# Kernel optimization log

Measured on AMD Instinct MI355X. Metric: run time of the kernel, lower is better.

The kernel has to match this reference:

```python
import jax, jax.numpy as jnp
import numpy as np

EPS = 0.001  # additive floor applied after relu, as in the torch code


def setup_inputs() -> dict:
    key = jax.random.key(0)
    kA, kB, kW = jax.random.split(key, 3)
    M, N, C, H, W = 512, 64, 128, 8, 8
    A = jax.random.normal(kA, (M, C, H, W), dtype=jnp.float32)
    B = jax.random.normal(kB, (N, C, H, W), dtype=jnp.float32)
    Wg = jax.random.normal(kW, (C, C), dtype=jnp.float32) * 0.01  # Wg.data.normal_(0.0, 0.01)
    return {"A": A, "B": B, "Wg": Wg}


def reference(A, B, Wg):
    # Faithful vectorization of MIMOcom.get_source_dst_max(A, B, dir=True).
    # Torch loops i,j over HxW: B0 = B[:, i, j, :]; G = B0 @ Wg;
    # combination[m, n, p] = sum_c A[m, p, c] * G[n, c]; running max over (i, j).
    M, C, H, W = A.shape
    N = B.shape[0]
    P = H * W
    Af = jnp.transpose(A, (0, 2, 3, 1)).reshape(M, P, C)  # [M, P, C]
    Bf = jnp.transpose(B, (0, 2, 3, 1)).reshape(N, P, C)  # [N, Q, C]
    G = Bf @ Wg                                           # [N, Q, D]
    scores = jnp.einsum('mpd,nqd->mnpq', Af, G)           # [M, N, P, Q]
    comb_max = scores.max(axis=-1)                        # max over B positions q
    return jax.nn.relu(comb_max) + EPS                    # [M, N, P]
```

## Files before the change

kernel.cpp:

```cpp
#include <hip/hip_runtime.h>
#include <hip/hip_bf16.h>
#include <stdint.h>

typedef __attribute__((ext_vector_type(8))) short bf16x8;
typedef __attribute__((ext_vector_type(16))) float f32x16;
using bf16 = __hip_bfloat16;

static constexpr int Mdim = 512;
static constexpr int Ndim = 64;
static constexpr int Cdim = 128;
static constexpr int Pdim = 64;
static constexpr float EPS_ADD = 0.001f;

#define SB0 __builtin_amdgcn_sched_barrier(0)

__global__ void prep_kernel(const float* __restrict__ A, const float* __restrict__ B,
                            const float* __restrict__ Wg,
                            bf16* __restrict__ Afrag, bf16* __restrict__ Gfrag) {
    __shared__ float lds[128 * 65];
    const int t = threadIdx.x;

    if (blockIdx.x < 512) {
        const int m = blockIdx.x;
        const float* __restrict__ Am = A + (size_t)m * (Cdim * Pdim);
#pragma unroll
        for (int i = 0; i < 8; ++i) {
            int v = t + i * 256;
            int gidx = v * 4;
            int c = gidx >> 6, p = gidx & 63;
            float4 val = *reinterpret_cast<const float4*>(Am + gidx);
            float* dst = &lds[c * 65 + p];
            dst[0] = val.x; dst[1] = val.y; dst[2] = val.z; dst[3] = val.w;
        }
        __syncthreads();

        unsigned* __restrict__ dst32 = (unsigned*)(Afrag + (size_t)m * 8192);
#pragma unroll
        for (int i = 0; i < 16; ++i) {
            int pr = t + i * 256;
            int p = pr >> 6;
            int c = (pr & 63) << 1;
            float f0 = lds[c * 65 + p];
            float f1 = lds[(c + 1) * 65 + p];
            union { bf16 hh[2]; unsigned u; } pk;
            pk.hh[0] = __float2bfloat16(f0);
            pk.hh[1] = __float2bfloat16(f1);
            int h = p >> 5, l31 = p & 31;
            int ks = c >> 4, hi = (c >> 3) & 1, e = c & 7;
            dst32[h * 2048 + ks * 256 + hi * 128 + l31 * 4 + (e >> 1)] = pk.u;
        }
    } else {
        const int nb = blockIdx.x - 512;
        const int n  = nb >> 2;
        const int q0 = (nb & 3) * 16;
        const float* __restrict__ Bn = B + (size_t)n * (Cdim * Pdim);
#pragma unroll
        for (int i = 0; i < 8; ++i) {
            int v = t + i * 256;
            int gidx = v * 4;
            int c = gidx >> 6, q = gidx & 63;
            float4 val = *reinterpret_cast<const float4*>(Bn + gidx);
            float* dst = &lds[c * 65 + q];
            dst[0] = val.x; dst[1] = val.y; dst[2] = val.z; dst[3] = val.w;
        }
        __syncthreads();

        const int d  = t & 127;
        const int qb = q0 + (t >> 7) * 8;
        float acc[8] = {0.f, 0.f, 0.f, 0.f, 0.f, 0.f, 0.f, 0.f};
        for (int c = 0; c < 128; ++c) {
            float w = Wg[c * 128 + d];
#pragma unroll
            for (int qi = 0; qi < 8; ++qi)
                acc[qi] = fmaf(lds[c * 65 + qb + qi], w, acc[qi]);
        }
        bf16* __restrict__ gdst = Gfrag + (size_t)n * 8192;
        const int ks = d >> 4, hi = (d >> 3) & 1, e = d & 7;
#pragma unroll
        for (int qi = 0; qi < 8; ++qi) {
            int q = qb + qi;
            int qt = q >> 5, l31 = q & 31;
            gdst[qt * 4096 + ks * 512 + hi * 256 + l31 * 8 + e] = __float2bfloat16(acc[qi]);
        }
    }
}

__global__ __launch_bounds__(256, 2)
void gemm_max_kernel(const bf16* __restrict__ Afrag, const bf16* __restrict__ Gfrag,
                     float* __restrict__ out) {
    const int tid  = threadIdx.x;
    const int lane = tid & 63;
    const int w    = tid >> 6;
    const int nw = w >> 1, h = w & 1;
    const int l31 = lane & 31, hi = lane >> 5;
    const int mg = blockIdx.x & 31;
    const int bn = blockIdx.x >> 5;
    const int n  = bn * 2 + nw;
    const int phase = bn & 15;

    bf16x8 gf[2][8];
    {
        const bf16* Gp = Gfrag + (size_t)n * 8192 + lane * 8;
#pragma unroll
        for (int qt = 0; qt < 2; ++qt)
#pragma unroll
            for (int ks = 0; ks < 8; ++ks)
                gf[qt][ks] = *reinterpret_cast<const bf16x8*>(Gp + qt * 4096 + ks * 512);
    }

    const bf16* Ab = Afrag + (size_t)mg * 16 * 8192 + h * 4096 + lane * 8;
    auto loadA = [&](bf16x8 (&dst)[8], int se) {
        const bf16* p = Ab + (size_t)se * 8192;
#pragma unroll
        for (int ks = 0; ks < 8; ++ks)
            dst[ks] = *reinterpret_cast<const bf16x8*>(p + ks * 512);
    };

    f32x16 acc0, acc1;
    const f32x16 z16 = {0.f,0.f,0.f,0.f,0.f,0.f,0.f,0.f,0.f,0.f,0.f,0.f,0.f,0.f,0.f,0.f};

    auto compute = [&](const bf16x8 (&a)[8]) {
#pragma unroll
        for (int ks = 0; ks < 8; ++ks) {
            acc0 = __builtin_amdgcn_mfma_f32_32x32x16_bf16(
                gf[0][ks], a[ks], ks == 0 ? z16 : acc0, 0, 0, 0);
            acc1 = __builtin_amdgcn_mfma_f32_32x32x16_bf16(
                gf[1][ks], a[ks], ks == 0 ? z16 : acc1, 0, 0, 0);
        }
    };

    auto epilogue = [&](int se) {
        float v01 = fmaxf(acc0[0], acc0[1]);
#pragma unroll
        for (int j = 2; j < 16; ++j) v01 = fmaxf(v01, acc0[j]);
        float v23 = fmaxf(acc1[0], acc1[1]);
#pragma unroll
        for (int j = 2; j < 16; ++j) v23 = fmaxf(v23, acc1[j]);
        float v = fmaxf(v01, v23);
        v = fmaxf(v, __shfl_xor(v, 32));
        if (hi == 0)
            out[(size_t)(mg * 16 + se) * 4096 + n * 64 + h * 32 + l31] =
                fmaxf(v, 0.f) + EPS_ADD;
    };

    bf16x8 aA[8], aB[8];
    loadA(aA, phase);

#pragma unroll
    for (int s = 0; s < 16; ++s) {
        const int se = (s + phase) & 15;
        const int sn = (s + 1 + phase) & 15;
        if ((s & 1) == 0) {
            if (s < 15) loadA(aB, sn);
            SB0;
            compute(aA);
            epilogue(se);
        } else {
            if (s < 15) loadA(aA, sn);
            SB0;
            compute(aB);
            epilogue(se);
        }
    }
}

extern "C" void kernel_launch(void* const* d_in, const int* in_sizes, int n_in,
                              void* d_out, int out_size, void* d_ws, size_t ws_size,
                              hipStream_t stream) {
    const float* A  = (const float*)d_in[0];
    const float* B  = (const float*)d_in[1];
    const float* Wg = (const float*)d_in[2];
    float* out = (float*)d_out;

    bf16* Afrag = (bf16*)d_ws;
    bf16* Gfrag = (bf16*)((char*)d_ws + (size_t)Mdim * Pdim * Cdim * sizeof(bf16));

    prep_kernel<<<768, 256, 0, stream>>>(A, B, Wg, Afrag, Gfrag);
    gemm_max_kernel<<<1024, 256, 0, stream>>>(Afrag, Gfrag, out);
}
```

Before: 55.83 us.

## Keep A fragments in registers and stream shared G tiles through LDS

The GEMM-max kernel is restructured so that each wave keeps one row m of A (both P halves) in registers and loops over 16 values of n. The G fragments for those n are staged into a double-buffered LDS tile with global_load_lds and shared by the block's four waves, instead of each wave reloading A from global memory. Synchronisation uses explicit vmcnt waits plus barriers, the grid is halved, and each step now issues four MFMAs per k-slice. The aim is less global/L2 traffic and better reuse of G. In exchange the kernel uses more LDS, and it depends on vmcnt ordering with the output stores.

```diff
diff --git a/kernel.cpp b/kernel.cpp
--- a/kernel.cpp
+++ b/kernel.cpp
@@ -13,6 +13,15 @@
 static constexpr float EPS_ADD = 0.001f;
 
 #define SB0 __builtin_amdgcn_sched_barrier(0)
+#define WAITV(N) asm volatile("s_waitcnt vmcnt(" #N ")" ::: "memory")
+
+__device__ __forceinline__ void gll16(const void* gsrc, void* ldst) {
+    const __attribute__((address_space(1))) unsigned int* g =
+        (const __attribute__((address_space(1))) unsigned int*)gsrc;
+    __attribute__((address_space(3))) unsigned int* l =
+        (__attribute__((address_space(3))) unsigned int*)(uintptr_t)ldst;
+    __builtin_amdgcn_global_load_lds(g, l, 16, 0, 0);
+}
 
 __global__ void prep_kernel(const float* __restrict__ A, const float* __restrict__ B,
                             const float* __restrict__ Wg,
@@ -88,79 +97,82 @@
 __global__ __launch_bounds__(256, 2)
 void gemm_max_kernel(const bf16* __restrict__ Afrag, const bf16* __restrict__ Gfrag,
                      float* __restrict__ out) {
+    __shared__ bf16 sG[2][8192];
     const int tid  = threadIdx.x;
     const int lane = tid & 63;
-    const int w    = tid >> 6;
-    const int nw = w >> 1, h = w & 1;
+    const int wv   = tid >> 6;
     const int l31 = lane & 31, hi = lane >> 5;
-    const int mg = blockIdx.x & 31;
-    const int bn = blockIdx.x >> 5;
-    const int n  = bn * 2 + nw;
-    const int phase = bn & 15;
+    const int mg = blockIdx.x & 127;
+    const int bn = blockIdx.x >> 7;
+    const int m  = mg * 4 + wv;
 
-    bf16x8 gf[2][8];
+    bf16x8 a[2][8];
     {
-        const bf16* Gp = Gfrag + (size_t)n * 8192 + lane * 8;
+        const bf16* Ap = Afrag + (size_t)m * 8192 + lane * 8;
+#pragma unroll
+        for (int h = 0; h < 2; ++h)
+#pragma unroll
+            for (int ks = 0; ks < 8; ++ks)
+                a[h][ks] = *reinterpret_cast<const bf16x8*>(Ap + h * 4096 + ks * 512);
+    }
+    asm volatile("" ::: "memory");
+
+    const char* Gsrc = (const char*)(Gfrag + (size_t)(bn * 16) * 8192);
+    auto stageG = [&](int s) {
+        char* dst = (char*)&sG[s & 1][0];
+        const char* src = Gsrc + (size_t)s * 16384;
+#pragma unroll
+        for (int i = 0; i < 4; ++i) {
+            int f = (i * 256 + tid) * 16;
+            gll16(src + f, dst + f);
+        }
+    };
+    stageG(0);
+
+    f32x16 acc[2][2];
+    const f32x16 z16 = {0.f,0.f,0.f,0.f,0.f,0.f,0.f,0.f,0.f,0.f,0.f,0.f,0.f,0.f,0.f,0.f};
+
+    auto compute = [&](int s) {
+        const char* gb = (const char*)&sG[s & 1][0] + lane * 16;
+        bf16x8 gf[2][8];
 #pragma unroll
         for (int qt = 0; qt < 2; ++qt)
 #pragma unroll
             for (int ks = 0; ks < 8; ++ks)
-                gf[qt][ks] = *reinterpret_cast<const bf16x8*>(Gp + qt * 4096 + ks * 512);
-    }
-
-    const bf16* Ab = Afrag + (size_t)mg * 16 * 8192 + h * 4096 + lane * 8;
-    auto loadA = [&](bf16x8 (&dst)[8], int se) {
-        const bf16* p = Ab + (size_t)se * 8192;
+                gf[qt][ks] = *reinterpret_cast<const bf16x8*>(gb + qt * 8192 + ks * 1024);
 #pragma unroll
         for (int ks = 0; ks < 8; ++ks)
-            dst[ks] = *reinterpret_cast<const bf16x8*>(p + ks * 512);
+#pragma unroll
+            for (int qt = 0; qt < 2; ++qt)
+#pragma unroll
+                for (int h = 0; h < 2; ++h)
+                    acc[qt][h] = __builtin_amdgcn_mfma_f32_32x32x16_bf16(
+                        gf[qt][ks], a[h][ks], ks == 0 ? z16 : acc[qt][h], 0, 0, 0);
     };
 
-    f32x16 acc0, acc1;
-    const f32x16 z16 = {0.f,0.f,0.f,0.f,0.f,0.f,0.f,0.f,0.f,0.f,0.f,0.f,0.f,0.f,0.f,0.f};
-
-    auto compute = [&](const bf16x8 (&a)[8]) {
+    auto epilogue = [&](int s) {
+        const int ng = bn * 16 + s;
 #pragma unroll
-        for (int ks = 0; ks < 8; ++ks) {
-            acc0 = __builtin_amdgcn_mfma_f32_32x32x16_bf16(
-                gf[0][ks], a[ks], ks == 0 ? z16 : acc0, 0, 0, 0);
-            acc1 = __builtin_amdgcn_mfma_f32_32x32x16_bf16(
-                gf[1][ks], a[ks], ks == 0 ? z16 : acc1, 0, 0, 0);
+        for (int h = 0; h < 2; ++h) {
+            float v = fmaxf(acc[0][h][0], acc[0][h][1]);
+#pragma unroll
+            for (int j = 2; j < 16; ++j) v = fmaxf(v, acc[0][h][j]);
+#pragma unroll
+            for (int j = 0; j < 16; ++j) v = fmaxf(v, acc[1][h][j]);
+            v = fmaxf(v, __shfl_xor(v, 32));
+            if (hi == 0)
+                out[(size_t)m * 4096 + ng * 64 + h * 32 + l31] = fmaxf(v, 0.f) + EPS_ADD;
         }
     };
 
-    auto epilogue = [&](int se) {
-        float v01 = fmaxf(acc0[0], acc0[1]);
-#pragma unroll
-        for (int j = 2; j < 16; ++j) v01 = fmaxf(v01, acc0[j]);
-        float v23 = fmaxf(acc1[0], acc1[1]);
-#pragma unroll
-        for (int j = 2; j < 16; ++j) v23 = fmaxf(v23, acc1[j]);
-        float v = fmaxf(v01, v23);
-        v = fmaxf(v, __shfl_xor(v, 32));
-        if (hi == 0)
-            out[(size_t)(mg * 16 + se) * 4096 + n * 64 + h * 32 + l31] =
-                fmaxf(v, 0.f) + EPS_ADD;
-    };
+    WAITV(0); __builtin_amdgcn_s_barrier(); SB0;
+    stageG(1);
+    compute(0); epilogue(0); SB0;
 
-    bf16x8 aA[8], aB[8];
-    loadA(aA, phase);
-
-#pragma unroll
-    for (int s = 0; s < 16; ++s) {
-        const int se = (s + phase) & 15;
-        const int sn = (s + 1 + phase) & 15;
-        if ((s & 1) == 0) {
-            if (s < 15) loadA(aB, sn);
-            SB0;
-            compute(aA);
-            epilogue(se);
-        } else {
-            if (s < 15) loadA(aA, sn);
-            SB0;
-            compute(aB);
-            epilogue(se);
-        }
+    for (int s = 1; s <= 15; ++s) {
+        WAITV(2); __builtin_amdgcn_s_barrier(); SB0;
+        if (s < 15) stageG(s + 1);
+        compute(s); epilogue(s); SB0;
     }
 }
 
@@ -176,5 +188,5 @@
     bf16* Gfrag = (bf16*)((char*)d_ws + (size_t)Mdim * Pdim * Cdim * sizeof(bf16));
 
     prep_kernel<<<768, 256, 0, stream>>>(A, B, Wg, Afrag, Gfrag);
-    gemm_max_kernel<<<1024, 256, 0, stream>>>(Afrag, Gfrag, out);
+    gemm_max_kernel<<<512, 256, 0, stream>>>(Afrag, Gfrag, out);
 }
```

New measurement: 46.08 us. 1.21x faster.
